# Kernel tuning notes

Measured on AMD Instinct MI355X. Metric: run time of the kernel, lower is better.

The kernel has to match this reference:

```python
import jax, jax.numpy as jnp
import numpy as np

HIDDEN = 2048
N_HEADS = 32
N_KV_HEADS = 8
N_GROUPS = N_HEADS // N_KV_HEADS  # 4
HEAD_DIM = HIDDEN // N_HEADS      # 64
BATCH, SEQ = 2, 2048


def setup_inputs() -> dict:
    key = jax.random.key(0)
    ks = jax.random.split(key, 5)
    s = 0.02
    return {
        "x": jax.random.normal(ks[0], (BATCH, SEQ, HIDDEN), dtype=jnp.float32),
        "Wq": jax.random.normal(ks[1], (HIDDEN, HIDDEN), dtype=jnp.float32) * s,
        "Wk": jax.random.normal(ks[2], (N_KV_HEADS * HEAD_DIM, HIDDEN), dtype=jnp.float32) * s,
        "Wv": jax.random.normal(ks[3], (N_KV_HEADS * HEAD_DIM, HIDDEN), dtype=jnp.float32) * s,
        "Wo": jax.random.normal(ks[4], (HIDDEN, HIDDEN), dtype=jnp.float32) * s,
    }


def reference(x, Wq, Wk, Wv, Wo):
    b, s, _ = x.shape
    # Projections (nn.Linear: y = x @ W.T)
    q = (x @ Wq.T).reshape(b, s, N_KV_HEADS, N_GROUPS, HEAD_DIM)  # group heads by kv head
    k = (x @ Wk.T).reshape(b, s, N_KV_HEADS, HEAD_DIM)
    v = (x @ Wv.T).reshape(b, s, N_KV_HEADS, HEAD_DIM)
    scale = 1.0 / jnp.sqrt(jnp.asarray(HEAD_DIM, dtype=x.dtype))
    # Grouped scores: equivalent to repeat_interleave of K over groups
    scores = jnp.einsum('bqhgd,bkhd->bhgqk', q, k) * scale  # [b, kvh, g, s, s]
    causal_mask = jnp.triu(jnp.ones((s, s), dtype=bool), k=1)
    scores = jnp.where(causal_mask, -jnp.inf, scores)
    attn = jax.nn.softmax(scores, axis=-1)
    out = jnp.einsum('bhgqk,bkhd->bqhgd', attn, v)  # [b, s, kvh, g, hd]
    out = out.reshape(b, s, HIDDEN)
    return out @ Wo.T
```

## Files before the change

### kernel.cpp

```cpp
#include <hip/hip_runtime.h>

#define HIDDEN 2048
#define NHEADS 32
#define NKV 8
#define HD 64
#define BATCH 2
#define SEQ 2048
#define MROWS (BATCH*SEQ)
#define KVDIM (NKV*HD)
#define QKVN (HIDDEN + 2*KVDIM)

typedef __bf16 bf16x8 __attribute__((ext_vector_type(8)));
typedef __bf16 bf16x4 __attribute__((ext_vector_type(4)));
typedef float f32x4 __attribute__((ext_vector_type(4)));
typedef short s16x4 __attribute__((ext_vector_type(4)));
typedef short s16x8 __attribute__((ext_vector_type(8)));

__device__ inline f32x4 mfma32(bf16x8 a, bf16x8 b, f32x4 c) {
    return __builtin_amdgcn_mfma_f32_16x16x32_bf16(a, b, c, 0, 0, 0);
}
__device__ inline f32x4 mfma16(s16x4 a, s16x4 b, f32x4 c) {
    return __builtin_amdgcn_mfma_f32_16x16x16bf16_1k(a, b, c, 0, 0, 0);
}

__device__ inline void gld16(const __bf16* g, __bf16* l) {
    __builtin_amdgcn_global_load_lds((const __attribute__((address_space(1))) void*)g,
                                     (__attribute__((address_space(3))) void*)l, 16, 0, 0);
}

__global__ __launch_bounds__(256) void cast_all(const float* __restrict__ x,
                                                const float* __restrict__ wq,
                                                const float* __restrict__ wk,
                                                const float* __restrict__ wv,
                                                const float* __restrict__ wo,
                                                __bf16* __restrict__ xb,
                                                __bf16* __restrict__ wqkv,
                                                __bf16* __restrict__ wob,
                                                float qscale) {
    int blk = blockIdx.x;
    const float* src; __bf16* dst; float sc = 1.0f; size_t off;
    if (blk < 8192)        { src = x;  dst = xb;   off = (size_t)blk * 1024; }
    else if (blk < 12288)  { src = wq; dst = wqkv; off = (size_t)(blk - 8192) * 1024; sc = qscale; }
    else if (blk < 13312)  { src = wk; dst = wqkv + (size_t)HIDDEN * HIDDEN; off = (size_t)(blk - 12288) * 1024; }
    else if (blk < 14336)  { src = wv; dst = wqkv + (size_t)(HIDDEN + KVDIM) * HIDDEN; off = (size_t)(blk - 13312) * 1024; }
    else                   { src = wo; dst = wob;  off = (size_t)(blk - 14336) * 1024; }
    size_t i4 = off + (size_t)threadIdx.x * 4;
    float4 f = *(const float4*)(src + i4);
    dst[i4 + 0] = (__bf16)(f.x * sc);
    dst[i4 + 1] = (__bf16)(f.y * sc);
    dst[i4 + 2] = (__bf16)(f.z * sc);
    dst[i4 + 3] = (__bf16)(f.w * sc);
}

__device__ inline void store_val(__bf16* C, size_t idx, float v) { C[idx] = (__bf16)v; }
__device__ inline void store_val(float* C, size_t idx, float v) { C[idx] = v; }

template <typename OutT>
__global__ __launch_bounds__(256) void gemm128(const __bf16* __restrict__ A,
                                               const __bf16* __restrict__ B,
                                               OutT* __restrict__ C,
                                               int M, int N, int K) {
    __shared__ __bf16 As[2][128][32];
    __shared__ __bf16 Bs[2][128][32];
    const int tid  = threadIdx.x;
    const int lane = tid & 63;
    const int w    = tid >> 6;
    const int col  = lane & 15;
    const int quad = lane >> 4;
    const int m0 = blockIdx.y * 128;
    const int n0 = blockIdx.x * 128;
    const int wm = (w >> 1) * 64;
    const int wn = (w & 1) * 64;

    f32x4 acc[4][4];
    #pragma unroll
    for (int i = 0; i < 4; i++)
        #pragma unroll
        for (int j = 0; j < 4; j++) acc[i][j] = (f32x4){0.f,0.f,0.f,0.f};

    const int lrow = lane >> 2;
    const int lcol = (lane & 3) * 8;

    auto stage = [&](int k0, int buf) {
        #pragma unroll
        for (int c = 0; c < 4; c++) {
            int chunk = w * 4 + c;
            if (chunk < 8) {
                const __bf16* g = A + (size_t)(m0 + chunk*16 + lrow) * K + k0 + lcol;
                gld16(g, &As[buf][chunk*16][0]);
            } else {
                int bc = chunk - 8;
                const __bf16* g = B + (size_t)(n0 + bc*16 + lrow) * K + k0 + lcol;
                gld16(g, &Bs[buf][bc*16][0]);
            }
        }
    };

    const int nk = K / 32;
    stage(0, 0);
    for (int ki = 0; ki < nk; ki++) {
        const int buf = ki & 1;
        __syncthreads();
        if (ki + 1 < nk) stage((ki + 1) * 32, buf ^ 1);

        bf16x8 af[4], bfr[4];
        #pragma unroll
        for (int i = 0; i < 4; i++) af[i]  = *(const bf16x8*)&As[buf][wm + i*16 + col][quad*8];
        #pragma unroll
        for (int j = 0; j < 4; j++) bfr[j] = *(const bf16x8*)&Bs[buf][wn + j*16 + col][quad*8];
        #pragma unroll
        for (int i = 0; i < 4; i++)
            #pragma unroll
            for (int j = 0; j < 4; j++)
                acc[i][j] = __builtin_amdgcn_mfma_f32_16x16x32_bf16(af[i], bfr[j], acc[i][j], 0, 0, 0);
    }

    #pragma unroll
    for (int i = 0; i < 4; i++) {
        #pragma unroll
        for (int r = 0; r < 4; r++) {
            int mrow = m0 + wm + i*16 + quad*4 + r;
            size_t base = (size_t)mrow * N + n0 + wn;
            #pragma unroll
            for (int j = 0; j < 4; j++)
                store_val(C, base + j*16 + col, acc[i][j][r]);
        }
    }
}

__global__ __launch_bounds__(256) void transpose_v(const __bf16* __restrict__ QKV,
                                                   __bf16* __restrict__ VT) {
    __shared__ __bf16 tile[64][72];
    const int r0 = blockIdx.x * 64;
    const int s0 = blockIdx.y * 64;
    const int t  = threadIdx.x;
    #pragma unroll
    for (int cc = 0; cc < 2; cc++) {
        int c = t + cc * 256;
        int i = c >> 3;
        int j8 = (c & 7) * 8;
        bf16x8 v = *(const bf16x8*)(QKV + (size_t)(s0 + i) * QKVN + (HIDDEN + KVDIM) + r0 + j8);
        *(bf16x8*)&tile[i][j8] = v;
    }
    __syncthreads();
    #pragma unroll
    for (int cc = 0; cc < 2; cc++) {
        int c = t + cc * 256;
        int d = c >> 3;
        int m = c & 7;
        bf16x8 vv;
        #pragma unroll
        for (int tt = 0; tt < 8; tt++) {
            int sl = (m >> 2) * 32 + (tt >> 2) * 16 + (m & 3) * 4 + (tt & 3);
            vv[tt] = tile[sl][d];
        }
        *(bf16x8*)(VT + (size_t)(r0 + d) * MROWS + s0 + m * 8) = vv;
    }
}

__global__ __launch_bounds__(256) void flash_attn(const __bf16* __restrict__ QKV,
                                                  const __bf16* __restrict__ VT,
                                                  __bf16* __restrict__ O) {
    const int bid  = blockIdx.x;
    const int p    = ((bid & 15) + 4 * ((bid >> 8) & 3)) & 15;
    const int head = (bid >> 4) & 31;
    const int b    = bid >> 9;
    const int kvh  = head >> 2;
    const int tid  = threadIdx.x;
    const int lane = tid & 63;
    const int w    = tid >> 6;
    const int col  = lane & 15;
    const int quad = lane >> 4;

    const int qbL = p * 64 + w * 16;
    const int qbH = (31 - p) * 64 + w * 16;
    const int np32 = (p + 1) * 2;
    const int nh32 = (32 - p) * 2;

    __shared__ __bf16 Ks[3][2][32][32];
    __shared__ __bf16 Vs[3][64][32];

    const size_t qL = (size_t)(b * SEQ + qbL + col) * QKVN + head * HD;
    const size_t qH = (size_t)(b * SEQ + qbH + col) * QKVN + head * HD;
    bf16x8 aqL0 = *(const bf16x8*)(QKV + qL + quad * 8);
    bf16x8 aqL1 = *(const bf16x8*)(QKV + qL + 32 + quad * 8);
    bf16x8 aqH0 = *(const bf16x8*)(QKV + qH + quad * 8);
    bf16x8 aqH1 = *(const bf16x8*)(QKV + qH + 32 + quad * 8);

    const s16x4 ones4 = { (short)0x3F80, (short)0x3F80, (short)0x3F80, (short)0x3F80 };

    f32x4 oL[4], oH[4];
    #pragma unroll
    for (int dn = 0; dn < 4; dn++) { oL[dn] = (f32x4){0.f,0.f,0.f,0.f}; oH[dn] = (f32x4){0.f,0.f,0.f,0.f}; }
    f32x4 lsumL = (f32x4){0.f,0.f,0.f,0.f};
    f32x4 lsumH = (f32x4){0.f,0.f,0.f,0.f};

    const int lrow = lane >> 2;
    const int srcc8 = (((lane & 3) ^ (lrow & 3)) * 8);
    const int swz   = (quad ^ (col & 3)) * 8;
    const size_t bS = (size_t)b * SEQ;

    const __bf16 *g0, *g1;
    size_t gstep;
    if (w < 2) {
        g0 = QKV + (bS + lrow) * QKVN + HIDDEN + kvh * HD + w * 32 + srcc8;
        g1 = g0 + (size_t)16 * QKVN;
        gstep = (size_t)32 * QKVN;
    } else {
        g0 = VT + (size_t)(kvh * HD + (w - 2) * 32 + lrow) * MROWS + bS + (lane & 3) * 8;
        g1 = g0 + (size_t)16 * MROWS;
        gstep = 32;
    }

    auto stage = [&](int sb) {
        if (w < 2) {
            gld16(g0, &Ks[sb][w][0][0]);
            gld16(g1, &Ks[sb][w][16][0]);
        } else {
            gld16(g0, &Vs[sb][(w - 2) * 32][0]);
            gld16(g1, &Vs[sb][(w - 2) * 32 + 16][0]);
        }
        g0 += gstep; g1 += gstep;
    };

    stage(0);
    stage(1);
    int cur = 0, nx2 = 2;
    for (int kt = 0; kt < nh32; kt++) {
        const int kbase = kt * 32;
        const bool dual = (kt < np32);
        if (kt + 1 < nh32) { __asm__ volatile("s_waitcnt vmcnt(2)" ::: "memory"); }
        else               { __asm__ volatile("s_waitcnt vmcnt(0)" ::: "memory"); }
        __builtin_amdgcn_s_barrier();
        __asm__ volatile("" ::: "memory");
        if (kt + 2 < nh32) stage(nx2);

        f32x4 sH[2], sL[2];
        #pragma unroll
        for (int j = 0; j < 2; j++) { sH[j] = (f32x4){0.f,0.f,0.f,0.f}; sL[j] = (f32x4){0.f,0.f,0.f,0.f}; }
        __builtin_amdgcn_s_setprio(1);
        #pragma unroll
        for (int j = 0; j < 2; j++) {
            bf16x8 bk0 = *(const bf16x8*)&Ks[cur][0][j*16 + col][swz];
            bf16x8 bk1 = *(const bf16x8*)&Ks[cur][1][j*16 + col][swz];
            sH[j] = mfma32(bk0, aqH0, sH[j]);
            sH[j] = mfma32(bk1, aqH1, sH[j]);
            if (dual) {
                sL[j] = mfma32(bk0, aqL0, sL[j]);
                sL[j] = mfma32(bk1, aqL1, sL[j]);
            }
        }
        __builtin_amdgcn_s_setprio(0);

        if (kt >= nh32 - 2) {
            #pragma unroll
            for (int j = 0; j < 2; j++)
                #pragma unroll
                for (int r = 0; r < 4; r++)
                    if (kbase + j*16 + quad*4 + r > qbH + col) sH[j][r] = -1e30f;
        }
        if (dual && kt >= np32 - 2) {
            #pragma unroll
            for (int j = 0; j < 2; j++)
                #pragma unroll
                for (int r = 0; r < 4; r++)
                    if (kbase + j*16 + quad*4 + r > qbL + col) sL[j][r] = -1e30f;
        }

        s16x4 paH[2], paL[2];
        #pragma unroll
        for (int j = 0; j < 2; j++) {
            bf16x4 tb;
            #pragma unroll
            for (int r = 0; r < 4; r++) tb[r] = (__bf16)__builtin_amdgcn_exp2f(sH[j][r]);
            paH[j] = __builtin_bit_cast(s16x4, tb);
            lsumH = mfma16(paH[j], ones4, lsumH);
        }
        if (dual) {
            #pragma unroll
            for (int j = 0; j < 2; j++) {
                bf16x4 tb;
                #pragma unroll
                for (int r = 0; r < 4; r++) tb[r] = (__bf16)__builtin_amdgcn_exp2f(sL[j][r]);
                paL[j] = __builtin_bit_cast(s16x4, tb);
                lsumL = mfma16(paL[j], ones4, lsumL);
            }
        }

        __builtin_amdgcn_s_setprio(1);
        #pragma unroll
        for (int dn = 0; dn < 4; dn++) {
            s16x8 bvv = *(const s16x8*)&Vs[cur][dn*16 + col][quad*8];
            s16x4 bv0 = __builtin_shufflevector(bvv, bvv, 0, 1, 2, 3);
            s16x4 bv1 = __builtin_shufflevector(bvv, bvv, 4, 5, 6, 7);
            oH[dn] = mfma16(paH[0], bv0, oH[dn]);
            oH[dn] = mfma16(paH[1], bv1, oH[dn]);
            if (dual) {
                oL[dn] = mfma16(paL[0], bv0, oL[dn]);
                oL[dn] = mfma16(paL[1], bv1, oL[dn]);
            }
        }
        __builtin_amdgcn_s_setprio(0);

        cur = (cur == 2) ? 0 : cur + 1;
        nx2 = (nx2 == 2) ? 0 : nx2 + 1;
    }

    #pragma unroll
    for (int r = 0; r < 4; r++) {
        float invL = 1.0f / lsumL[r];
        float invH = 1.0f / lsumH[r];
        __bf16* opL = O + (size_t)(b * SEQ + qbL + quad*4 + r) * HIDDEN + head * HD;
        __bf16* opH = O + (size_t)(b * SEQ + qbH + quad*4 + r) * HIDDEN + head * HD;
        #pragma unroll
        for (int dn = 0; dn < 4; dn++) {
            opL[dn*16 + col] = (__bf16)(oL[dn][r] * invL);
            opH[dn*16 + col] = (__bf16)(oH[dn][r] * invH);
        }
    }
}

extern "C" void kernel_launch(void* const* d_in, const int* in_sizes, int n_in,
                              void* d_out, int out_size, void* d_ws, size_t ws_size,
                              hipStream_t stream) {
    const float* x  = (const float*)d_in[0];
    const float* Wq = (const float*)d_in[1];
    const float* Wk = (const float*)d_in[2];
    const float* Wv = (const float*)d_in[3];
    const float* Wo = (const float*)d_in[4];
    float* out = (float*)d_out;

    __bf16* p    = (__bf16*)d_ws;
    __bf16* xb   = p; p += (size_t)MROWS * HIDDEN;
    __bf16* wqkv = p; p += (size_t)QKVN * HIDDEN;
    __bf16* wob  = p; p += (size_t)HIDDEN * HIDDEN;
    __bf16* qkv  = p; p += (size_t)MROWS * QKVN;
    __bf16* vt   = p; p += (size_t)KVDIM * MROWS;
    __bf16* aob  = xb;

    const float qscale = 0.125f * 1.4426950408889634f;
    cast_all<<<18432, 256, 0, stream>>>(x, Wq, Wk, Wv, Wo, xb, wqkv, wob, qscale);

    dim3 blk(256);
    gemm128<__bf16><<<dim3(QKVN/128, MROWS/128), blk, 0, stream>>>(xb, wqkv, qkv, MROWS, QKVN, HIDDEN);
    transpose_v<<<dim3(KVDIM/64, MROWS/64), blk, 0, stream>>>(qkv, vt);
    flash_attn<<<BATCH * NHEADS * (SEQ/128), blk, 0, stream>>>(qkv, vt, aob);
    gemm128<float><<<dim3(HIDDEN/128, MROWS/128), blk, 0, stream>>>(aob, wob, out, MROWS, HIDDEN, HIDDEN);
}
```

Before: 312.7 us.

## Replace paired low/high query tiles with one tile per block, heaviest-first ordering

```diff
diff --git a/kernel.cpp b/kernel.cpp
--- a/kernel.cpp
+++ b/kernel.cpp
@@ -13,14 +13,9 @@
 typedef __bf16 bf16x8 __attribute__((ext_vector_type(8)));
 typedef __bf16 bf16x4 __attribute__((ext_vector_type(4)));
 typedef float f32x4 __attribute__((ext_vector_type(4)));
-typedef short s16x4 __attribute__((ext_vector_type(4)));
-typedef short s16x8 __attribute__((ext_vector_type(8)));
 
 __device__ inline f32x4 mfma32(bf16x8 a, bf16x8 b, f32x4 c) {
     return __builtin_amdgcn_mfma_f32_16x16x32_bf16(a, b, c, 0, 0, 0);
-}
-__device__ inline f32x4 mfma16(s16x4 a, s16x4 b, f32x4 c) {
-    return __builtin_amdgcn_mfma_f32_16x16x16bf16_1k(a, b, c, 0, 0, 0);
 }
 
 __device__ inline void gld16(const __bf16* g, __bf16* l) {
@@ -162,9 +157,9 @@
                                                   const __bf16* __restrict__ VT,
                                                   __bf16* __restrict__ O) {
     const int bid  = blockIdx.x;
-    const int p    = ((bid & 15) + 4 * ((bid >> 8) & 3)) & 15;
-    const int head = (bid >> 4) & 31;
-    const int b    = bid >> 9;
+    const int t    = 31 - (bid >> 6);
+    const int head = (bid >> 1) & 31;
+    const int b    = bid & 1;
     const int kvh  = head >> 2;
     const int tid  = threadIdx.x;
     const int lane = tid & 63;
@@ -172,28 +167,24 @@
     const int col  = lane & 15;
     const int quad = lane >> 4;
 
-    const int qbL = p * 64 + w * 16;
-    const int qbH = (31 - p) * 64 + w * 16;
-    const int np32 = (p + 1) * 2;
-    const int nh32 = (32 - p) * 2;
+    const int qb   = t * 64 + w * 16;
+    const int n32  = (t + 1) * 2;
 
     __shared__ __bf16 Ks[3][2][32][32];
     __shared__ __bf16 Vs[3][64][32];
 
-    const size_t qL = (size_t)(b * SEQ + qbL + col) * QKVN + head * HD;
-    const size_t qH = (size_t)(b * SEQ + qbH + col) * QKVN + head * HD;
-    bf16x8 aqL0 = *(const bf16x8*)(QKV + qL + quad * 8);
-    bf16x8 aqL1 = *(const bf16x8*)(QKV + qL + 32 + quad * 8);
-    bf16x8 aqH0 = *(const bf16x8*)(QKV + qH + quad * 8);
-    bf16x8 aqH1 = *(const bf16x8*)(QKV + qH + 32 + quad * 8);
-
-    const s16x4 ones4 = { (short)0x3F80, (short)0x3F80, (short)0x3F80, (short)0x3F80 };
-
-    f32x4 oL[4], oH[4];
-    #pragma unroll
-    for (int dn = 0; dn < 4; dn++) { oL[dn] = (f32x4){0.f,0.f,0.f,0.f}; oH[dn] = (f32x4){0.f,0.f,0.f,0.f}; }
-    f32x4 lsumL = (f32x4){0.f,0.f,0.f,0.f};
-    f32x4 lsumH = (f32x4){0.f,0.f,0.f,0.f};
+    const size_t qO = (size_t)(b * SEQ + qb + col) * QKVN + head * HD;
+    bf16x8 aq0 = *(const bf16x8*)(QKV + qO + quad * 8);
+    bf16x8 aq1 = *(const bf16x8*)(QKV + qO + 32 + quad * 8);
+
+    bf16x8 ones8;
+    #pragma unroll
+    for (int j = 0; j < 8; j++) ones8[j] = (__bf16)1.0f;
+
+    f32x4 o[4];
+    #pragma unroll
+    for (int dn = 0; dn < 4; dn++) o[dn] = (f32x4){0.f,0.f,0.f,0.f};
+    f32x4 lsum = (f32x4){0.f,0.f,0.f,0.f};
 
     const int lrow = lane >> 2;
     const int srcc8 = (((lane & 3) ^ (lrow & 3)) * 8);
@@ -226,79 +217,48 @@
     stage(0);
     stage(1);
     int cur = 0, nx2 = 2;
-    for (int kt = 0; kt < nh32; kt++) {
+    for (int kt = 0; kt < n32; kt++) {
         const int kbase = kt * 32;
-        const bool dual = (kt < np32);
-        if (kt + 1 < nh32) { __asm__ volatile("s_waitcnt vmcnt(2)" ::: "memory"); }
-        else               { __asm__ volatile("s_waitcnt vmcnt(0)" ::: "memory"); }
+        if (kt + 1 < n32) { __asm__ volatile("s_waitcnt vmcnt(2)" ::: "memory"); }
+        else              { __asm__ volatile("s_waitcnt vmcnt(0)" ::: "memory"); }
         __builtin_amdgcn_s_barrier();
         __asm__ volatile("" ::: "memory");
-        if (kt + 2 < nh32) stage(nx2);
-
-        f32x4 sH[2], sL[2];
-        #pragma unroll
-        for (int j = 0; j < 2; j++) { sH[j] = (f32x4){0.f,0.f,0.f,0.f}; sL[j] = (f32x4){0.f,0.f,0.f,0.f}; }
+        if (kt + 2 < n32) stage(nx2);
+
+        f32x4 s[2];
+        s[0] = (f32x4){0.f,0.f,0.f,0.f};
+        s[1] = (f32x4){0.f,0.f,0.f,0.f};
         __builtin_amdgcn_s_setprio(1);
         #pragma unroll
         for (int j = 0; j < 2; j++) {
             bf16x8 bk0 = *(const bf16x8*)&Ks[cur][0][j*16 + col][swz];
             bf16x8 bk1 = *(const bf16x8*)&Ks[cur][1][j*16 + col][swz];
-            sH[j] = mfma32(bk0, aqH0, sH[j]);
-            sH[j] = mfma32(bk1, aqH1, sH[j]);
-            if (dual) {
-                sL[j] = mfma32(bk0, aqL0, sL[j]);
-                sL[j] = mfma32(bk1, aqL1, sL[j]);
-            }
+            s[j] = mfma32(bk0, aq0, s[j]);
+            s[j] = mfma32(bk1, aq1, s[j]);
         }
         __builtin_amdgcn_s_setprio(0);
 
-        if (kt >= nh32 - 2) {
+        if (kt >= n32 - 2) {
             #pragma unroll
             for (int j = 0; j < 2; j++)
                 #pragma unroll
                 for (int r = 0; r < 4; r++)
-                    if (kbase + j*16 + quad*4 + r > qbH + col) sH[j][r] = -1e30f;
-        }
-        if (dual && kt >= np32 - 2) {
+                    if (kbase + j*16 + quad*4 + r > qb + col) s[j][r] = -1e30f;
+        }
+
+        bf16x8 pa;
+        #pragma unroll
+        for (int j = 0; j < 2; j++)
             #pragma unroll
-            for (int j = 0; j < 2; j++)
-                #pragma unroll
-                for (int r = 0; r < 4; r++)
-                    if (kbase + j*16 + quad*4 + r > qbL + col) sL[j][r] = -1e30f;
-        }
-
-        s16x4 paH[2], paL[2];
-        #pragma unroll
-        for (int j = 0; j < 2; j++) {
-            bf16x4 tb;
-            #pragma unroll
-            for (int r = 0; r < 4; r++) tb[r] = (__bf16)__builtin_amdgcn_exp2f(sH[j][r]);
-            paH[j] = __builtin_bit_cast(s16x4, tb);
-            lsumH = mfma16(paH[j], ones4, lsumH);
-        }
-        if (dual) {
-            #pragma unroll
-            for (int j = 0; j < 2; j++) {
-                bf16x4 tb;
-                #pragma unroll
-                for (int r = 0; r < 4; r++) tb[r] = (__bf16)__builtin_amdgcn_exp2f(sL[j][r]);
-                paL[j] = __builtin_bit_cast(s16x4, tb);
-                lsumL = mfma16(paL[j], ones4, lsumL);
-            }
-        }
+            for (int r = 0; r < 4; r++)
+                pa[j*4 + r] = (__bf16)__builtin_amdgcn_exp2f(s[j][r]);
 
         __builtin_amdgcn_s_setprio(1);
+        lsum = mfma32(pa, ones8, lsum);
         #pragma unroll
         for (int dn = 0; dn < 4; dn++) {
-            s16x8 bvv = *(const s16x8*)&Vs[cur][dn*16 + col][quad*8];
-            s16x4 bv0 = __builtin_shufflevector(bvv, bvv, 0, 1, 2, 3);
-            s16x4 bv1 = __builtin_shufflevector(bvv, bvv, 4, 5, 6, 7);
-            oH[dn] = mfma16(paH[0], bv0, oH[dn]);
-            oH[dn] = mfma16(paH[1], bv1, oH[dn]);
-            if (dual) {
-                oL[dn] = mfma16(paL[0], bv0, oL[dn]);
-                oL[dn] = mfma16(paL[1], bv1, oL[dn]);
-            }
+            bf16x8 bv = *(const bf16x8*)&Vs[cur][dn*16 + col][quad*8];
+            o[dn] = mfma32(pa, bv, o[dn]);
         }
         __builtin_amdgcn_s_setprio(0);
 
@@ -308,15 +268,11 @@
 
     #pragma unroll
     for (int r = 0; r < 4; r++) {
-        float invL = 1.0f / lsumL[r];
-        float invH = 1.0f / lsumH[r];
-        __bf16* opL = O + (size_t)(b * SEQ + qbL + quad*4 + r) * HIDDEN + head * HD;
-        __bf16* opH = O + (size_t)(b * SEQ + qbH + quad*4 + r) * HIDDEN + head * HD;
-        #pragma unroll
-        for (int dn = 0; dn < 4; dn++) {
-            opL[dn*16 + col] = (__bf16)(oL[dn][r] * invL);
-            opH[dn*16 + col] = (__bf16)(oH[dn][r] * invH);
-        }
+        float inv = 1.0f / lsum[r];
+        __bf16* op = O + (size_t)(b * SEQ + qb + quad*4 + r) * HIDDEN + head * HD;
+        #pragma unroll
+        for (int dn = 0; dn < 4; dn++)
+            op[dn*16 + col] = (__bf16)(o[dn][r] * inv);
     }
 }
 
@@ -344,6 +300,6 @@
     dim3 blk(256);
     gemm128<__bf16><<<dim3(QKVN/128, MROWS/128), blk, 0, stream>>>(xb, wqkv, qkv, MROWS, QKVN, HIDDEN);
     transpose_v<<<dim3(KVDIM/64, MROWS/64), blk, 0, stream>>>(qkv, vt);
-    flash_attn<<<BATCH * NHEADS * (SEQ/128), blk, 0, stream>>>(qkv, vt, aob);
+    flash_attn<<<BATCH * NHEADS * (SEQ/64), blk, 0, stream>>>(qkv, vt, aob);
     gemm128<float><<<dim3(HIDDEN/128, MROWS/128), blk, 0, stream>>>(aob, wob, out, MROWS, HIDDEN, HIDDEN);
 }
```

New measurement: 283.9 us. -9.2%, faster.
